# Kernel tuning notes

Hardware: AMD Instinct MI355X
Metric: run time of the kernel (lower is better)

Reference implementation:

```python
import jax, jax.numpy as jnp
import numpy as np

SIZE = (512, 512, 256)  # voxel grid dims (x, y, z)
N_PTS = 2_000_000       # number of query points


def setup_inputs() -> dict:
    key = jax.random.key(0)
    k1, k2 = jax.random.split(key)
    lower = jnp.array([-4.0, -4.0, -1.0], jnp.float32)
    resolution = jnp.array([64.0, 64.0, 64.0], jnp.float32)
    # physical extent of the grid along each axis
    extent = (jnp.array(SIZE, jnp.float32) - 1.0) / resolution
    x = (lower - 0.05 * extent) + jax.random.uniform(k1, (N_PTS, 3), jnp.float32) * (1.1 * extent)
    # learned parameter: hk.get_parameter('grid', (*size, 2)); random instead of zeros so outputs are nontrivial
    grid = jax.random.normal(k2, (*SIZE, 2), jnp.float32) * 0.1
    return {"x": x, "grid": grid, "lower": lower, "resolution": resolution}


def _trilinear(index, grid):
    """index: [N,3] float grid coords; grid: [X,Y,Z,2] -> [N,2]."""
    size = jnp.array(grid.shape[:3], jnp.int32)
    c0f = jnp.floor(index)
    f = index - c0f            # fractional offsets, [N,3]
    c0 = c0f.astype(jnp.int32)  # lower corner, [N,3]
    out = jnp.zeros((index.shape[0], grid.shape[-1]), grid.dtype)
    for dx in (0, 1):
        for dy in (0, 1):
            for dz in (0, 1):
                w = ((f[:, 0] if dx else 1.0 - f[:, 0])
                     * (f[:, 1] if dy else 1.0 - f[:, 1])
                     * (f[:, 2] if dz else 1.0 - f[:, 2]))
                ix = jnp.clip(c0[:, 0] + dx, 0, size[0] - 1)
                iy = jnp.clip(c0[:, 1] + dy, 0, size[1] - 1)
                iz = jnp.clip(c0[:, 2] + dz, 0, size[2] - 1)
                out = out + w[:, None] * grid[ix, iy, iz]  # gather [N,2]
    return out


def reference(x, grid, lower, resolution):
    size = jnp.array(grid.shape[:3], jnp.float32)
    index = (x - lower) * resolution               # [N,3] continuous grid coords
    valid = jnp.all((index >= 0.0) & (index <= size - 1.0), axis=-1)  # [N]
    vals = jnp.where(valid[:, None], _trilinear(index, grid), 0.0)    # [N,2]
    sigma, alpha = vals[:, 0], vals[:, 1]
    return sigma, alpha
```

## Files before the change

### kernel.cpp

```cpp
#include <hip/hip_runtime.h>

#define NX 512
#define NY 512
#define NZ 256

__global__ __launch_bounds__(256) void trilerp_kernel(
    const float* __restrict__ x,
    const float* __restrict__ grid,
    const float* __restrict__ lower,
    const float* __restrict__ resolution,
    float* __restrict__ out,
    int n)
{
    int i = blockIdx.x * blockDim.x + threadIdx.x;
    if (i >= n) return;

    float px = x[3 * i + 0];
    float py = x[3 * i + 1];
    float pz = x[3 * i + 2];

    float lx = lower[0], ly = lower[1], lz = lower[2];
    float rx = resolution[0], ry = resolution[1], rz = resolution[2];

    float fx = (px - lx) * rx;
    float fy = (py - ly) * ry;
    float fz = (pz - lz) * rz;

    bool valid = (fx >= 0.0f) && (fx <= (float)(NX - 1)) &&
                 (fy >= 0.0f) && (fy <= (float)(NY - 1)) &&
                 (fz >= 0.0f) && (fz <= (float)(NZ - 1));

    float sigma = 0.0f, alpha = 0.0f;

    if (valid) {
        float cfx = floorf(fx), cfy = floorf(fy), cfz = floorf(fz);
        float wx = fx - cfx, wy = fy - cfy, wz = fz - cfz;

        int ix0 = (int)cfx, iy0 = (int)cfy, iz0 = (int)cfz;
        int ix1 = min(ix0 + 1, NX - 1);
        int iy1 = min(iy0 + 1, NY - 1);
        int iz1 = min(iz0 + 1, NZ - 1);

        const float2* __restrict__ g = (const float2*)grid;

        int b00 = (ix0 * NY + iy0) * NZ;
        int b01 = (ix0 * NY + iy1) * NZ;
        int b10 = (ix1 * NY + iy0) * NZ;
        int b11 = (ix1 * NY + iy1) * NZ;

        float2 v000 = g[b00 + iz0];
        float2 v001 = g[b00 + iz1];
        float2 v010 = g[b01 + iz0];
        float2 v011 = g[b01 + iz1];
        float2 v100 = g[b10 + iz0];
        float2 v101 = g[b10 + iz1];
        float2 v110 = g[b11 + iz0];
        float2 v111 = g[b11 + iz1];

        float ux = 1.0f - wx, uy = 1.0f - wy, uz = 1.0f - wz;

        float w000 = ux * uy * uz;
        float w001 = ux * uy * wz;
        float w010 = ux * wy * uz;
        float w011 = ux * wy * wz;
        float w100 = wx * uy * uz;
        float w101 = wx * uy * wz;
        float w110 = wx * wy * uz;
        float w111 = wx * wy * wz;

        sigma = w000 * v000.x + w001 * v001.x + w010 * v010.x + w011 * v011.x +
                w100 * v100.x + w101 * v101.x + w110 * v110.x + w111 * v111.x;
        alpha = w000 * v000.y + w001 * v001.y + w010 * v010.y + w011 * v011.y +
                w100 * v100.y + w101 * v101.y + w110 * v110.y + w111 * v111.y;
    }

    out[i] = sigma;
    out[n + i] = alpha;
}

extern "C" void kernel_launch(void* const* d_in, const int* in_sizes, int n_in,
                              void* d_out, int out_size, void* d_ws, size_t ws_size,
                              hipStream_t stream) {
    const float* x          = (const float*)d_in[0];
    const float* grid       = (const float*)d_in[1];
    const float* lower      = (const float*)d_in[2];
    const float* resolution = (const float*)d_in[3];
    float* out              = (float*)d_out;

    int n = in_sizes[0] / 3;

    int block = 256;
    int blocks = (n + block - 1) / block;
    trilerp_kernel<<<blocks, block, 0, stream>>>(x, grid, lower, resolution, out, n);
}
```

Baseline: 713.7 us.

## Process two points per thread with 16-byte paired-z gathers and vector stores

```diff
diff --git a/kernel.cpp b/kernel.cpp
--- a/kernel.cpp
+++ b/kernel.cpp
@@ -4,7 +4,56 @@
 #define NY 512
 #define NZ 256
 
-__global__ __launch_bounds__(256) void trilerp_kernel(
+typedef float v4f __attribute__((ext_vector_type(4)));
+
+struct PtPrep {
+    int b00, b01, b10, b11;
+    float wx, wy, wz;
+    bool valid;
+};
+
+__device__ __forceinline__ PtPrep prep(float px, float py, float pz,
+                                       float lx, float ly, float lz,
+                                       float rx, float ry, float rz) {
+    PtPrep r;
+    float fx = (px - lx) * rx;
+    float fy = (py - ly) * ry;
+    float fz = (pz - lz) * rz;
+    r.valid = (fx >= 0.0f) && (fx <= (float)(NX - 1)) &&
+              (fy >= 0.0f) && (fy <= (float)(NY - 1)) &&
+              (fz >= 0.0f) && (fz <= (float)(NZ - 1));
+    int ix0 = min(max((int)floorf(fx), 0), NX - 2);
+    int iy0 = min(max((int)floorf(fy), 0), NY - 2);
+    int iz0 = min(max((int)floorf(fz), 0), NZ - 2);
+    r.wx = fx - (float)ix0;
+    r.wy = fy - (float)iy0;
+    r.wz = fz - (float)iz0;
+    int row0 = (ix0 * NY + iy0) * NZ + iz0;
+    r.b00 = r.valid ? row0 : 0;
+    r.b01 = r.valid ? row0 + NZ : 0;
+    r.b10 = r.valid ? row0 + NY * NZ : 0;
+    r.b11 = r.valid ? row0 + NY * NZ + NZ : 0;
+    return r;
+}
+
+__device__ __forceinline__ void finish(const v4f& v00, const v4f& v01,
+                                       const v4f& v10, const v4f& v11,
+                                       const PtPrep& p, float& sigma, float& alpha) {
+    float uz = 1.0f - p.wz, uy = 1.0f - p.wy, ux = 1.0f - p.wx;
+    float s00 = v00.x * uz + v00.z * p.wz;
+    float a00 = v00.y * uz + v00.w * p.wz;
+    float s01 = v01.x * uz + v01.z * p.wz;
+    float a01 = v01.y * uz + v01.w * p.wz;
+    float s10 = v10.x * uz + v10.z * p.wz;
+    float a10 = v10.y * uz + v10.w * p.wz;
+    float s11 = v11.x * uz + v11.z * p.wz;
+    float a11 = v11.y * uz + v11.w * p.wz;
+    sigma = ux * (uy * s00 + p.wy * s01) + p.wx * (uy * s10 + p.wy * s11);
+    alpha = ux * (uy * a00 + p.wy * a01) + p.wx * (uy * a10 + p.wy * a11);
+    if (!p.valid) { sigma = 0.0f; alpha = 0.0f; }
+}
+
+__global__ __launch_bounds__(256) void trilerp2_kernel(
     const float* __restrict__ x,
     const float* __restrict__ grid,
     const float* __restrict__ lower,
@@ -12,70 +61,48 @@
     float* __restrict__ out,
     int n)
 {
-    int i = blockIdx.x * blockDim.x + threadIdx.x;
-    if (i >= n) return;
-
-    float px = x[3 * i + 0];
-    float py = x[3 * i + 1];
-    float pz = x[3 * i + 2];
+    int t = blockIdx.x * blockDim.x + threadIdx.x;
+    int i0 = 2 * t;
+    if (i0 >= n) return;
+    bool has2 = (i0 + 1) < n;
 
     float lx = lower[0], ly = lower[1], lz = lower[2];
     float rx = resolution[0], ry = resolution[1], rz = resolution[2];
 
-    float fx = (px - lx) * rx;
-    float fy = (py - ly) * ry;
-    float fz = (pz - lz) * rz;
+    const float* xp = x + 6 * (size_t)t;
+    float2 d0 = *(const float2*)xp;
+    float p0x = d0.x, p0y = d0.y;
+    float p0z = xp[2];
+    float p1x = 0.0f, p1y = 0.0f, p1z = 0.0f;
+    if (has2) { p1x = xp[3]; p1y = xp[4]; p1z = xp[5]; }
 
-    bool valid = (fx >= 0.0f) && (fx <= (float)(NX - 1)) &&
-                 (fy >= 0.0f) && (fy <= (float)(NY - 1)) &&
-                 (fz >= 0.0f) && (fz <= (float)(NZ - 1));
+    PtPrep q0 = prep(p0x, p0y, p0z, lx, ly, lz, rx, ry, rz);
+    PtPrep q1 = prep(p1x, p1y, p1z, lx, ly, lz, rx, ry, rz);
 
-    float sigma = 0.0f, alpha = 0.0f;
+    const float2* g = (const float2*)grid;
 
-    if (valid) {
-        float cfx = floorf(fx), cfy = floorf(fy), cfz = floorf(fz);
-        float wx = fx - cfx, wy = fy - cfy, wz = fz - cfz;
+    v4f A00, A01, A10, A11, B00, B01, B10, B11;
+    __builtin_memcpy(&A00, g + q0.b00, 16);
+    __builtin_memcpy(&A01, g + q0.b01, 16);
+    __builtin_memcpy(&A10, g + q0.b10, 16);
+    __builtin_memcpy(&A11, g + q0.b11, 16);
+    __builtin_memcpy(&B00, g + q1.b00, 16);
+    __builtin_memcpy(&B01, g + q1.b01, 16);
+    __builtin_memcpy(&B10, g + q1.b10, 16);
+    __builtin_memcpy(&B11, g + q1.b11, 16);
 
-        int ix0 = (int)cfx, iy0 = (int)cfy, iz0 = (int)cfz;
-        int ix1 = min(ix0 + 1, NX - 1);
-        int iy1 = min(iy0 + 1, NY - 1);
-        int iz1 = min(iz0 + 1, NZ - 1);
+    float s0, a0, s1, a1;
+    finish(A00, A01, A10, A11, q0, s0, a0);
+    finish(B00, B01, B10, B11, q1, s1, a1);
 
-        const float2* __restrict__ g = (const float2*)grid;
-
-        int b00 = (ix0 * NY + iy0) * NZ;
-        int b01 = (ix0 * NY + iy1) * NZ;
-        int b10 = (ix1 * NY + iy0) * NZ;
-        int b11 = (ix1 * NY + iy1) * NZ;
-
-        float2 v000 = g[b00 + iz0];
-        float2 v001 = g[b00 + iz1];
-        float2 v010 = g[b01 + iz0];
-        float2 v011 = g[b01 + iz1];
-        float2 v100 = g[b10 + iz0];
-        float2 v101 = g[b10 + iz1];
-        float2 v110 = g[b11 + iz0];
-        float2 v111 = g[b11 + iz1];
-
-        float ux = 1.0f - wx, uy = 1.0f - wy, uz = 1.0f - wz;
-
-        float w000 = ux * uy * uz;
-        float w001 = ux * uy * wz;
-        float w010 = ux * wy * uz;
-        float w011 = ux * wy * wz;
-        float w100 = wx * uy * uz;
-        float w101 = wx * uy * wz;
-        float w110 = wx * wy * uz;
-        float w111 = wx * wy * wz;
-
-        sigma = w000 * v000.x + w001 * v001.x + w010 * v010.x + w011 * v011.x +
-                w100 * v100.x + w101 * v101.x + w110 * v110.x + w111 * v111.x;
-        alpha = w000 * v000.y + w001 * v001.y + w010 * v010.y + w011 * v011.y +
-                w100 * v100.y + w101 * v101.y + w110 * v110.y + w111 * v111.y;
+    if (has2 && ((n & 1) == 0)) {
+        *(float2*)(out + i0)     = make_float2(s0, s1);
+        *(float2*)(out + n + i0) = make_float2(a0, a1);
+    } else {
+        out[i0] = s0;
+        out[n + i0] = a0;
+        if (has2) { out[i0 + 1] = s1; out[n + i0 + 1] = a1; }
     }
-
-    out[i] = sigma;
-    out[n + i] = alpha;
 }
 
 extern "C" void kernel_launch(void* const* d_in, const int* in_sizes, int n_in,
@@ -88,8 +115,8 @@
     float* out              = (float*)d_out;
 
     int n = in_sizes[0] / 3;
-
+    int threads = (n + 1) / 2;
     int block = 256;
-    int blocks = (n + block - 1) / block;
-    trilerp_kernel<<<blocks, block, 0, stream>>>(x, grid, lower, resolution, out, n);
+    int blocks = (threads + block - 1) / block;
+    trilerp2_kernel<<<blocks, block, 0, stream>>>(x, grid, lower, resolution, out, n);
 }
```

Result: no change. 716.0 us (+0.3%).
